# Kernel optimization log

Measured on AMD Instinct MI355X. Metric: run time of the kernel, lower is better.

Reference implementation:

```python
import jax, jax.numpy as jnp
import numpy as np

B, C_CLS, D_WORD, J = 1024, 80, 300, 8000
IMG_CH = 2048

def setup_inputs() -> dict:
    key = jax.random.key(0)
    ks = jax.random.split(key, 9)
    return {
        'feature': jax.random.normal(ks[0], (B, IMG_CH), jnp.float32),
        'inp': jax.random.normal(ks[1], (1, C_CLS, D_WORD), jnp.float32),
        'A': jax.random.uniform(ks[2], (C_CLS, C_CLS), jnp.float32),
        'W_gc1': jax.random.normal(ks[3], (D_WORD, 1024), jnp.float32) * (1.0 / np.sqrt(1024)),
        'W_gc2': jax.random.normal(ks[4], (1024, 2048), jnp.float32) * (1.0 / np.sqrt(2048)),
        'W_img': jax.random.normal(ks[5], (J, IMG_CH), jnp.float32) * 0.02,
        'b_img': jax.random.normal(ks[6], (J,), jnp.float32) * 0.02,
        'W_cls': jax.random.normal(ks[7], (J, 2048), jnp.float32) * 0.02,
        'b_cls': jax.random.normal(ks[8], (J,), jnp.float32) * 0.02,
    }

def _gen_adj(A):
    # torch: D = A.sum(1)**-0.5; adj = (A @ diag(D)).T @ diag(D) = D[:,None]*A.T*D[None,:]
    D = jnp.power(jnp.sum(A, axis=1), -0.5)
    return D[:, None] * A.T * D[None, :]

def reference(feature, inp, A, W_gc1, W_gc2, W_img, b_img, W_cls, b_cls):
    inp0 = inp[0]                                   # [C, 300]
    adj = jax.lax.stop_gradient(_gen_adj(A))        # [C, C], .detach() in torch
    x = adj @ (inp0 @ W_gc1)                        # gc1: [C, 1024]
    x = jax.nn.leaky_relu(x, negative_slope=0.2)
    x = adj @ (x @ W_gc2)                           # gc2: [C, 2048]
    # MFB bilinear pooling (is_usemfb=True, is_hash=False -> out_in_tmp=1, eval-mode dropout=identity)
    # original: out[b,c] = sum_j (Linear_img(feature[b])[j] * Linear_cls(x_col_c)[j])
    img_proj = feature @ W_img.T + b_img            # [B, J]
    cls_proj = x @ W_cls.T + b_cls                  # [C, J]
    x_out = img_proj @ cls_proj.T                   # [B, C]
    return x_out
```

## Files before the change

### kernel.cpp

```cpp
#include <hip/hip_runtime.h>
#include <hip/hip_bf16.h>


typedef __bf16 bf16_t;
typedef __bf16 bf16x8 __attribute__((ext_vector_type(8)));
typedef float f32x4 __attribute__((ext_vector_type(4)));

#define MFMA16(a, b, c) __builtin_amdgcn_mfma_f32_16x16x32_bf16((a), (b), (c), 0, 0, 0)

#define GLOAD_LDS16(g, l)                                     \
  __builtin_amdgcn_global_load_lds(                           \
      (const __attribute__((address_space(1))) void*)(g),     \
      (__attribute__((address_space(3))) void*)(l), 16, 0, 0)

#define PIN()                                   \
  do {                                          \
    asm volatile("" ::: "memory");              \
    __builtin_amdgcn_sched_barrier(0);          \
  } while (0)

#define BARRIER()                               \
  do {                                          \
    PIN();                                      \
    __builtin_amdgcn_s_barrier();               \
    PIN();                                      \
  } while (0)

__device__ inline bf16x8 cvt8(float4 a, float4 b) {
  bf16x8 v;
  v[0] = (bf16_t)a.x; v[1] = (bf16_t)a.y; v[2] = (bf16_t)a.z; v[3] = (bf16_t)a.w;
  v[4] = (bf16_t)b.x; v[5] = (bf16_t)b.y; v[6] = (bf16_t)b.z; v[7] = (bf16_t)b.w;
  return v;
}

__global__ void k_adj(const float* __restrict__ A, float* __restrict__ adj) {
  __shared__ float Dv[80];
  int tid = threadIdx.x;
  if (tid < 80) {
    float s = 0.f;
    #pragma unroll 4
    for (int j = 0; j < 80; ++j) s += A[tid * 80 + j];
    Dv[tid] = rsqrtf(s);
  }
  __syncthreads();
  for (int idx = tid; idx < 6400; idx += blockDim.x) {
    int i = idx / 80, j = idx % 80;
    adj[idx] = Dv[i] * Dv[j] * A[j * 80 + i];
  }
}

__global__ void k_cvt0(const float* __restrict__ inp0, bf16_t* __restrict__ x0b) {
  int idx = blockIdx.x * blockDim.x + threadIdx.x;
  if (idx < 30720) {
    int c = idx / 384, k = idx % 384;
    x0b[idx] = (k < 300) ? (bf16_t)inp0[c * 300 + k] : (bf16_t)0.f;
  }
}

__global__ __launch_bounds__(256) void k_gc1m(
    const bf16_t* __restrict__ x0b, const float* __restrict__ Wgc1,
    float* __restrict__ t1) {
  int tid = threadIdx.x;
  int w = tid >> 6, l = tid & 63;
  int ln = l & 15, q = l >> 4;
  int n0 = blockIdx.x * 16;

  __shared__ float red[4][80][16];
  f32x4 acc[5] = {};
  for (int ks = 0; ks < 3; ++ks) {
    int kq = w * 96 + ks * 32 + q * 8;
    bf16x8 bfrag;
    #pragma unroll
    for (int jj = 0; jj < 8; ++jj) {
      int k = kq + jj;
      int kc = k < 300 ? k : 299;
      float wv = Wgc1[kc * 1024 + n0 + ln];
      bfrag[jj] = (bf16_t)(k < 300 ? wv : 0.f);
    }
    #pragma unroll
    for (int mt = 0; mt < 5; ++mt) {
      bf16x8 afrag = *(const bf16x8*)(x0b + (size_t)(mt * 16 + ln) * 384 + kq);
      acc[mt] = MFMA16(afrag, bfrag, acc[mt]);
    }
  }
  #pragma unroll
  for (int mt = 0; mt < 5; ++mt)
    #pragma unroll
    for (int reg = 0; reg < 4; ++reg)
      red[w][mt * 16 + q * 4 + reg][ln] = acc[mt][reg];
  __syncthreads();
  for (int o = tid; o < 1280; o += 256) {
    int c = o >> 4, nn = o & 15;
    t1[c * 1024 + n0 + nn] = red[0][c][nn] + red[1][c][nn] + red[2][c][nn] + red[3][c][nn];
  }
}

__global__ void k_adjmul_leaky(const float* __restrict__ adj, const float* __restrict__ t1,
                               bf16_t* __restrict__ x1b) {
  int idx = blockIdx.x * blockDim.x + threadIdx.x;
  int c = idx >> 10, n = idx & 1023;
  const float* ar = adj + c * 80;
  float acc = 0.f;
  #pragma unroll 4
  for (int cc = 0; cc < 80; ++cc) acc += ar[cc] * t1[cc * 1024 + n];
  x1b[idx] = (bf16_t)(acc > 0.f ? acc : 0.2f * acc);
}

__global__ __launch_bounds__(256) void k_gc2m(
    const bf16_t* __restrict__ x1b, const float* __restrict__ Wgc2,
    float* __restrict__ t2) {
  int tid = threadIdx.x;
  int w = tid >> 6, l = tid & 63;
  int ln = l & 15, q = l >> 4;
  int nc = blockIdx.x & 31, kc = blockIdx.x >> 5;

  __shared__ float BsF[2 * 2048];
  auto stage = [&](int b, int k0) {
    #pragma unroll
    for (int it = 0; it < 2; ++it) {
      int slot = tid + it * 256;
      int kr = slot >> 4, nq = slot & 15;
      const float* src = Wgc2 + (size_t)(k0 + kr) * 2048 + nc * 64 + nq * 4;
      float* dst = BsF + b * 2048 + slot * 4;
      GLOAD_LDS16(src, dst);
    }
  };

  int kb = kc * 64;
  bf16x8 a0[5], a1[5];
  #pragma unroll
  for (int mt = 0; mt < 5; ++mt)
    a0[mt] = *(const bf16x8*)(x1b + (size_t)(mt * 16 + ln) * 1024 + kb + q * 8);
  PIN();
  stage(0, kb);
  PIN();
  stage(1, kb + 32);
  PIN();
  #pragma unroll
  for (int mt = 0; mt < 5; ++mt)
    a1[mt] = *(const bf16x8*)(x1b + (size_t)(mt * 16 + ln) * 1024 + kb + 32 + q * 8);
  PIN();

  f32x4 acc[5] = {};
  asm volatile("s_waitcnt vmcnt(7)" ::: "memory");
  BARRIER();
  {
    bf16x8 bfrag;
    #pragma unroll
    for (int jj = 0; jj < 8; ++jj) bfrag[jj] = (bf16_t)BsF[(q * 8 + jj) * 64 + w * 16 + ln];
    #pragma unroll
    for (int mt = 0; mt < 5; ++mt) acc[mt] = MFMA16(a0[mt], bfrag, acc[mt]);
  }
  asm volatile("s_waitcnt vmcnt(5)" ::: "memory");
  BARRIER();
  {
    bf16x8 bfrag;
    #pragma unroll
    for (int jj = 0; jj < 8; ++jj)
      bfrag[jj] = (bf16_t)BsF[2048 + (q * 8 + jj) * 64 + w * 16 + ln];
    #pragma unroll
    for (int mt = 0; mt < 5; ++mt) acc[mt] = MFMA16(a1[mt], bfrag, acc[mt]);
  }

  #pragma unroll
  for (int mt = 0; mt < 5; ++mt)
    #pragma unroll
    for (int reg = 0; reg < 4; ++reg)
      atomicAdd(&t2[(size_t)(mt * 16 + q * 4 + reg) * 2048 + nc * 64 + w * 16 + ln],
                acc[mt][reg]);
}

__global__ void k_adjmul_bf16(const float* __restrict__ adj, const float* __restrict__ t2,
                              bf16_t* __restrict__ x2) {
  int idx = blockIdx.x * blockDim.x + threadIdx.x;
  int c = idx >> 11, n = idx & 2047;
  const float* ar = adj + c * 80;
  float acc = 0.f;
  #pragma unroll 4
  for (int cc = 0; cc < 80; ++cc) acc += ar[cc] * t2[cc * 2048 + n];
  x2[idx] = (bf16_t)acc;
}

__global__ __launch_bounds__(256) void k_clsproj(
    const float* __restrict__ Wcls, const float* __restrict__ bcls,
    const float* __restrict__ bimg, const bf16_t* __restrict__ x2,
    bf16_t* __restrict__ P, float* __restrict__ r) {
  int tid = threadIdx.x;
  int w = tid >> 6, l = tid & 63;
  int ln = l & 15, q = l >> 4;
  int j0 = blockIdx.x * 16;
  size_t jrow = (size_t)(j0 + ln) * 2048;

  __shared__ float red[4][80][16];
  __shared__ float rloc[80];
  if (tid < 80) rloc[tid] = 0.f;

  f32x4 acc[5] = {};
  int kbase = w * 512 + q * 8;
  for (int ks = 0; ks < 16; ++ks) {
    int kq = kbase + ks * 32;
    const float4* bp = (const float4*)(Wcls + jrow + kq);
    float4 b0 = bp[0], b1 = bp[1];
    bf16x8 bfrag = cvt8(b0, b1);
    #pragma unroll
    for (int mt = 0; mt < 5; ++mt) {
      bf16x8 afrag = *(const bf16x8*)(x2 + (size_t)(mt * 16 + ln) * 2048 + kq);
      acc[mt] = MFMA16(afrag, bfrag, acc[mt]);
    }
  }
  #pragma unroll
  for (int mt = 0; mt < 5; ++mt)
    #pragma unroll
    for (int reg = 0; reg < 4; ++reg)
      red[w][mt * 16 + q * 4 + reg][ln] = acc[mt][reg];
  __syncthreads();

  for (int o = tid; o < 1280; o += 256) {
    int c = o >> 4, jj = o & 15;
    float v = red[0][c][jj] + red[1][c][jj] + red[2][c][jj] + red[3][c][jj] + bcls[j0 + jj];
    P[(size_t)c * 8000 + j0 + jj] = (bf16_t)v;
    atomicAdd(&rloc[c], bimg[j0 + jj] * v);
  }
  __syncthreads();
  if (tid < 80) atomicAdd(&r[tid], rloc[tid]);
}

__global__ __launch_bounds__(256) void k_hmat(
    const float* __restrict__ Wimg, const bf16_t* __restrict__ P, float* __restrict__ H) {
  int tid = threadIdx.x;
  int w = tid >> 6, l = tid & 63;
  int ln = l & 15, q = l >> 4;
  int jc = blockIdx.x >> 4, ncg = blockIdx.x & 15;
  int jbase = jc * 320;
  int n0 = (ncg * 4 + w) * 32;

  __shared__ float Bs[4 * 3 * 1024];
  float* Bw = Bs + w * 3072;

  auto stage = [&](int buf, int jt) {
    #pragma unroll
    for (int it = 0; it < 4; ++it) {
      int row = it * 8 + (l >> 3);
      const float* src = Wimg + (size_t)(jt + row) * 2048 + n0 + (l & 7) * 4;
      float* dst = Bw + buf * 1024 + it * 256 + l * 4;
      GLOAD_LDS16(src, dst);
    }
  };
  auto loadA = [&](bf16x8* a, int j0) {
    #pragma unroll
    for (int mt = 0; mt < 5; ++mt)
      a[mt] = *(const bf16x8*)(P + (size_t)(mt * 16 + ln) * 8000 + j0 + q * 8);
  };

  f32x4 acc[5][2] = {};
  bf16x8 aCur[5], aNxt[5];

  loadA(aCur, jbase);
  PIN();
  stage(0, jbase);
  PIN();
  stage(1, jbase + 32);
  PIN();

  #pragma unroll
  for (int s = 0; s < 10; ++s) {
    if (s < 9) {
      loadA(aNxt, jbase + (s + 1) * 32);
      PIN();
    }
    if (s < 8) {
      stage((s + 2) % 3, jbase + (s + 2) * 32);
      PIN();
    }
    if (s < 8)       asm volatile("s_waitcnt vmcnt(13)" ::: "memory");
    else if (s == 8) asm volatile("s_waitcnt vmcnt(9)"  ::: "memory");
    else             asm volatile("s_waitcnt vmcnt(5)"  ::: "memory");
    PIN();
    const float* Bc = Bw + (s % 3) * 1024;
    bf16x8 bfrag[2];
    #pragma unroll
    for (int nt = 0; nt < 2; ++nt)
      #pragma unroll
      for (int jj = 0; jj < 8; ++jj)
        bfrag[nt][jj] = (bf16_t)Bc[(q * 8 + jj) * 32 + nt * 16 + ln];
    #pragma unroll
    for (int mt = 0; mt < 5; ++mt)
      #pragma unroll
      for (int nt = 0; nt < 2; ++nt)
        acc[mt][nt] = MFMA16(aCur[mt], bfrag[nt], acc[mt][nt]);
    PIN();
    if (s < 9) {
      #pragma unroll
      for (int mt = 0; mt < 5; ++mt) aCur[mt] = aNxt[mt];
    }
  }

  #pragma unroll
  for (int mt = 0; mt < 5; ++mt)
    #pragma unroll
    for (int nt = 0; nt < 2; ++nt)
      #pragma unroll
      for (int reg = 0; reg < 4; ++reg)
        atomicAdd(&H[(size_t)(mt * 16 + q * 4 + reg) * 2048 + n0 + nt * 16 + ln],
                  acc[mt][nt][reg]);
}

__global__ __launch_bounds__(256) void k_out(
    const float* __restrict__ feat, const float* __restrict__ H,
    const float* __restrict__ r, float* __restrict__ out) {
  int tid = threadIdx.x;
  int w = tid >> 6, l = tid & 63;
  int ln = l & 15, q = l >> 4;
  int mg = blockIdx.x & 15, kc = blockIdx.x >> 4;
  int m0 = mg * 64 + w * 16;
  size_t frow = (size_t)(m0 + ln) * 2048;

  f32x4 acc[5] = {};
  int kbase = kc * 64 + q * 8;
  #pragma unroll
  for (int ks = 0; ks < 2; ++ks) {
    int kq = kbase + ks * 32;
    const float4* ap = (const float4*)(feat + frow + kq);
    bf16x8 afrag = cvt8(ap[0], ap[1]);
    #pragma unroll
    for (int nt = 0; nt < 5; ++nt) {
      const float4* hp = (const float4*)(H + (size_t)(nt * 16 + ln) * 2048 + kq);
      bf16x8 bfrag = cvt8(hp[0], hp[1]);
      acc[nt] = MFMA16(afrag, bfrag, acc[nt]);
    }
  }
  #pragma unroll
  for (int nt = 0; nt < 5; ++nt)
    #pragma unroll
    for (int reg = 0; reg < 4; ++reg) {
      int b = m0 + q * 4 + reg;
      int c = nt * 16 + ln;
      float v = acc[nt][reg];
      if (kc == 0) v += r[c];
      atomicAdd(&out[b * 80 + c], v);
    }
}

extern "C" void kernel_launch(void* const* d_in, const int* in_sizes, int n_in,
                              void* d_out, int out_size, void* d_ws, size_t ws_size,
                              hipStream_t stream) {
  const float* feature = (const float*)d_in[0];
  const float* inp     = (const float*)d_in[1];
  const float* A       = (const float*)d_in[2];
  const float* Wgc1    = (const float*)d_in[3];
  const float* Wgc2    = (const float*)d_in[4];
  const float* Wimg    = (const float*)d_in[5];
  const float* bimg    = (const float*)d_in[6];
  const float* Wcls    = (const float*)d_in[7];
  const float* bcls    = (const float*)d_in[8];
  float* out = (float*)d_out;

  char* ws = (char*)d_ws;
  float*  adj = (float*)(ws + 0);
  float*  t1  = (float*)(ws + 25600);
  bf16_t* x1b = (bf16_t*)(ws + 353280);
  float*  t2  = (float*)(ws + 517120);
  bf16_t* x2  = (bf16_t*)(ws + 1172480);
  bf16_t* P   = (bf16_t*)(ws + 1500160);
  float*  H   = (float*)(ws + 2780160);
  float*  r   = (float*)(ws + 3435520);
  bf16_t* x0b = (bf16_t*)(ws + 3435840);

  hipMemsetAsync(t2, 0, 80 * 2048 * 4, stream);
  hipMemsetAsync(H, 0, 80 * 2048 * 4, stream);
  hipMemsetAsync(r, 0, 80 * 4, stream);
  hipMemsetAsync(out, 0, 1024 * 80 * 4, stream);

  k_adj<<<1, 128, 0, stream>>>(A, adj);
  k_cvt0<<<120, 256, 0, stream>>>(inp, x0b);
  k_gc1m<<<64, 256, 0, stream>>>(x0b, Wgc1, t1);
  k_adjmul_leaky<<<320, 256, 0, stream>>>(adj, t1, x1b);
  k_gc2m<<<512, 256, 0, stream>>>(x1b, Wgc2, t2);
  k_adjmul_bf16<<<640, 256, 0, stream>>>(adj, t2, x2);
  k_clsproj<<<500, 256, 0, stream>>>(Wcls, bcls, bimg, x2, P, r);
  k_hmat<<<400, 256, 0, stream>>>(Wimg, P, H);
  k_out<<<512, 256, 0, stream>>>(feature, H, r, out);
}
```

Before: 271.8 us.

## Split-K gc1 and hmat across more blocks, software-pipeline clsproj loads

```diff
diff --git a/kernel.cpp b/kernel.cpp
--- a/kernel.cpp
+++ b/kernel.cpp
@@ -19,13 +19,6 @@
     __builtin_amdgcn_sched_barrier(0);          \
   } while (0)
 
-#define BARRIER()                               \
-  do {                                          \
-    PIN();                                      \
-    __builtin_amdgcn_s_barrier();               \
-    PIN();                                      \
-  } while (0)
-
 __device__ inline bf16x8 cvt8(float4 a, float4 b) {
   bf16x8 v;
   v[0] = (bf16_t)a.x; v[1] = (bf16_t)a.y; v[2] = (bf16_t)a.z; v[3] = (bf16_t)a.w;
@@ -57,31 +50,30 @@
   }
 }
 
-__global__ __launch_bounds__(256) void k_gc1m(
+__global__ __launch_bounds__(256, 2) void k_gc1m(
     const bf16_t* __restrict__ x0b, const float* __restrict__ Wgc1,
     float* __restrict__ t1) {
   int tid = threadIdx.x;
   int w = tid >> 6, l = tid & 63;
   int ln = l & 15, q = l >> 4;
-  int n0 = blockIdx.x * 16;
+  int n0 = (blockIdx.x & 63) * 16;
+  int kc = blockIdx.x >> 6;
+  int kq = kc * 128 + w * 32 + q * 8;
 
   __shared__ float red[4][80][16];
   f32x4 acc[5] = {};
-  for (int ks = 0; ks < 3; ++ks) {
-    int kq = w * 96 + ks * 32 + q * 8;
-    bf16x8 bfrag;
-    #pragma unroll
-    for (int jj = 0; jj < 8; ++jj) {
-      int k = kq + jj;
-      int kc = k < 300 ? k : 299;
-      float wv = Wgc1[kc * 1024 + n0 + ln];
-      bfrag[jj] = (bf16_t)(k < 300 ? wv : 0.f);
-    }
-    #pragma unroll
-    for (int mt = 0; mt < 5; ++mt) {
-      bf16x8 afrag = *(const bf16x8*)(x0b + (size_t)(mt * 16 + ln) * 384 + kq);
-      acc[mt] = MFMA16(afrag, bfrag, acc[mt]);
-    }
+  bf16x8 bfrag;
+  #pragma unroll
+  for (int jj = 0; jj < 8; ++jj) {
+    int k = kq + jj;
+    int kcl = k < 300 ? k : 299;
+    float wv = Wgc1[kcl * 1024 + n0 + ln];
+    bfrag[jj] = (bf16_t)(k < 300 ? wv : 0.f);
+  }
+  #pragma unroll
+  for (int mt = 0; mt < 5; ++mt) {
+    bf16x8 afrag = *(const bf16x8*)(x0b + (size_t)(mt * 16 + ln) * 384 + kq);
+    acc[mt] = MFMA16(afrag, bfrag, acc[mt]);
   }
   #pragma unroll
   for (int mt = 0; mt < 5; ++mt)
@@ -91,7 +83,8 @@
   __syncthreads();
   for (int o = tid; o < 1280; o += 256) {
     int c = o >> 4, nn = o & 15;
-    t1[c * 1024 + n0 + nn] = red[0][c][nn] + red[1][c][nn] + red[2][c][nn] + red[3][c][nn];
+    atomicAdd(&t1[c * 1024 + n0 + nn],
+              red[0][c][nn] + red[1][c][nn] + red[2][c][nn] + red[3][c][nn]);
   }
 }
 
@@ -106,7 +99,7 @@
   x1b[idx] = (bf16_t)(acc > 0.f ? acc : 0.2f * acc);
 }
 
-__global__ __launch_bounds__(256) void k_gc2m(
+__global__ __launch_bounds__(256, 2) void k_gc2m(
     const bf16_t* __restrict__ x1b, const float* __restrict__ Wgc2,
     float* __restrict__ t2) {
   int tid = threadIdx.x;
@@ -143,7 +136,9 @@
 
   f32x4 acc[5] = {};
   asm volatile("s_waitcnt vmcnt(7)" ::: "memory");
-  BARRIER();
+  PIN();
+  __builtin_amdgcn_s_barrier();
+  PIN();
   {
     bf16x8 bfrag;
     #pragma unroll
@@ -152,7 +147,9 @@
     for (int mt = 0; mt < 5; ++mt) acc[mt] = MFMA16(a0[mt], bfrag, acc[mt]);
   }
   asm volatile("s_waitcnt vmcnt(5)" ::: "memory");
-  BARRIER();
+  PIN();
+  __builtin_amdgcn_s_barrier();
+  PIN();
   {
     bf16x8 bfrag;
     #pragma unroll
@@ -181,7 +178,7 @@
   x2[idx] = (bf16_t)acc;
 }
 
-__global__ __launch_bounds__(256) void k_clsproj(
+__global__ __launch_bounds__(256, 2) void k_clsproj(
     const float* __restrict__ Wcls, const float* __restrict__ bcls,
     const float* __restrict__ bimg, const bf16_t* __restrict__ x2,
     bf16_t* __restrict__ P, float* __restrict__ r) {
@@ -197,16 +194,30 @@
 
   f32x4 acc[5] = {};
   int kbase = w * 512 + q * 8;
+
+  float4 bA[2], bB[2];
+  bf16x8 aF[2][5];
+  {
+    const float4* bp = (const float4*)(Wcls + jrow + kbase);
+    bA[0] = bp[0]; bB[0] = bp[1];
+    #pragma unroll
+    for (int mt = 0; mt < 5; ++mt)
+      aF[0][mt] = *(const bf16x8*)(x2 + (size_t)(mt * 16 + ln) * 2048 + kbase);
+  }
+  #pragma unroll
   for (int ks = 0; ks < 16; ++ks) {
-    int kq = kbase + ks * 32;
-    const float4* bp = (const float4*)(Wcls + jrow + kq);
-    float4 b0 = bp[0], b1 = bp[1];
-    bf16x8 bfrag = cvt8(b0, b1);
-    #pragma unroll
-    for (int mt = 0; mt < 5; ++mt) {
-      bf16x8 afrag = *(const bf16x8*)(x2 + (size_t)(mt * 16 + ln) * 2048 + kq);
-      acc[mt] = MFMA16(afrag, bfrag, acc[mt]);
-    }
+    int cur = ks & 1, nxt = cur ^ 1;
+    if (ks < 15) {
+      int kq = kbase + (ks + 1) * 32;
+      const float4* bp = (const float4*)(Wcls + jrow + kq);
+      bA[nxt] = bp[0]; bB[nxt] = bp[1];
+      #pragma unroll
+      for (int mt = 0; mt < 5; ++mt)
+        aF[nxt][mt] = *(const bf16x8*)(x2 + (size_t)(mt * 16 + ln) * 2048 + kq);
+    }
+    bf16x8 bfrag = cvt8(bA[cur], bB[cur]);
+    #pragma unroll
+    for (int mt = 0; mt < 5; ++mt) acc[mt] = MFMA16(aF[cur][mt], bfrag, acc[mt]);
   }
   #pragma unroll
   for (int mt = 0; mt < 5; ++mt)
@@ -225,13 +236,13 @@
   if (tid < 80) atomicAdd(&r[tid], rloc[tid]);
 }
 
-__global__ __launch_bounds__(256) void k_hmat(
+__global__ __launch_bounds__(256, 2) void k_hmat(
     const float* __restrict__ Wimg, const bf16_t* __restrict__ P, float* __restrict__ H) {
   int tid = threadIdx.x;
   int w = tid >> 6, l = tid & 63;
   int ln = l & 15, q = l >> 4;
   int jc = blockIdx.x >> 4, ncg = blockIdx.x & 15;
-  int jbase = jc * 320;
+  int jbase = jc * 160;
   int n0 = (ncg * 4 + w) * 32;
 
   __shared__ float Bs[4 * 3 * 1024];
@@ -246,16 +257,16 @@
       GLOAD_LDS16(src, dst);
     }
   };
-  auto loadA = [&](bf16x8* a, int j0) {
+  auto loadA = [&](bf16x8* a, int jt) {
     #pragma unroll
     for (int mt = 0; mt < 5; ++mt)
-      a[mt] = *(const bf16x8*)(P + (size_t)(mt * 16 + ln) * 8000 + j0 + q * 8);
+      a[mt] = *(const bf16x8*)(P + (size_t)(mt * 16 + ln) * 8000 + jt + q * 8);
   };
 
   f32x4 acc[5][2] = {};
-  bf16x8 aCur[5], aNxt[5];
-
-  loadA(aCur, jbase);
+  bf16x8 aF[2][5];
+
+  loadA(aF[0], jbase);
   PIN();
   stage(0, jbase);
   PIN();
@@ -263,17 +274,17 @@
   PIN();
 
   #pragma unroll
-  for (int s = 0; s < 10; ++s) {
-    if (s < 9) {
-      loadA(aNxt, jbase + (s + 1) * 32);
+  for (int s = 0; s < 5; ++s) {
+    if (s < 4) {
+      loadA(aF[(s + 1) & 1], jbase + (s + 1) * 32);
       PIN();
     }
-    if (s < 8) {
+    if (s < 3) {
       stage((s + 2) % 3, jbase + (s + 2) * 32);
       PIN();
     }
-    if (s < 8)       asm volatile("s_waitcnt vmcnt(13)" ::: "memory");
-    else if (s == 8) asm volatile("s_waitcnt vmcnt(9)"  ::: "memory");
+    if (s < 3)       asm volatile("s_waitcnt vmcnt(13)" ::: "memory");
+    else if (s == 3) asm volatile("s_waitcnt vmcnt(9)"  ::: "memory");
     else             asm volatile("s_waitcnt vmcnt(5)"  ::: "memory");
     PIN();
     const float* Bc = Bw + (s % 3) * 1024;
@@ -287,12 +298,8 @@
     for (int mt = 0; mt < 5; ++mt)
       #pragma unroll
       for (int nt = 0; nt < 2; ++nt)
-        acc[mt][nt] = MFMA16(aCur[mt], bfrag[nt], acc[mt][nt]);
+        acc[mt][nt] = MFMA16(aF[s & 1][mt], bfrag[nt], acc[mt][nt]);
     PIN();
-    if (s < 9) {
-      #pragma unroll
-      for (int mt = 0; mt < 5; ++mt) aCur[mt] = aNxt[mt];
-    }
   }
 
   #pragma unroll
@@ -305,7 +312,7 @@
                   acc[mt][nt][reg]);
 }
 
-__global__ __launch_bounds__(256) void k_out(
+__global__ __launch_bounds__(256, 2) void k_out(
     const float* __restrict__ feat, const float* __restrict__ H,
     const float* __restrict__ r, float* __restrict__ out) {
   int tid = threadIdx.x;
@@ -366,6 +373,7 @@
   float*  r   = (float*)(ws + 3435520);
   bf16_t* x0b = (bf16_t*)(ws + 3435840);
 
+  hipMemsetAsync(t1, 0, 80 * 1024 * 4, stream);
   hipMemsetAsync(t2, 0, 80 * 2048 * 4, stream);
   hipMemsetAsync(H, 0, 80 * 2048 * 4, stream);
   hipMemsetAsync(r, 0, 80 * 4, stream);
@@ -373,11 +381,11 @@
 
   k_adj<<<1, 128, 0, stream>>>(A, adj);
   k_cvt0<<<120, 256, 0, stream>>>(inp, x0b);
-  k_gc1m<<<64, 256, 0, stream>>>(x0b, Wgc1, t1);
+  k_gc1m<<<192, 256, 0, stream>>>(x0b, Wgc1, t1);
   k_adjmul_leaky<<<320, 256, 0, stream>>>(adj, t1, x1b);
   k_gc2m<<<512, 256, 0, stream>>>(x1b, Wgc2, t2);
   k_adjmul_bf16<<<640, 256, 0, stream>>>(adj, t2, x2);
   k_clsproj<<<500, 256, 0, stream>>>(Wcls, bcls, bimg, x2, P, r);
-  k_hmat<<<400, 256, 0, stream>>>(Wimg, P, H);
+  k_hmat<<<800, 256, 0, stream>>>(Wimg, P, H);
   k_out<<<512, 256, 0, stream>>>(feature, H, r, out);
 }
```

After: 287.1 us. 1.06x slower.
